# Performance work log

Hardware: AMD Instinct MI355X
Metric: run time of the kernel (lower is better)

The kernel has to match this reference:

```python
import jax, jax.numpy as jnp
import numpy as np

N = 50000
E = 800000
IN_DIM = 256
HID = 256
OUT_DIM = 2


def setup_inputs() -> dict:
    key = jax.random.key(0)
    ks = jax.random.split(key, 10)
    x = jax.random.normal(ks[0], (N, IN_DIM), dtype=jnp.float32)
    edge_index = jax.random.randint(ks[1], (2, E), 0, N, dtype=jnp.int64)
    # Glorot-ish scaling so activations stay well-conditioned through 4 layers
    def w(k, fan_in, fan_out):
        return jax.random.normal(k, (fan_in, fan_out), dtype=jnp.float32) / jnp.sqrt(jnp.float32(fan_in))
    return {
        "x": x,
        "edge_index": edge_index,
        "W0": w(ks[2], IN_DIM, HID), "b0": jnp.zeros((HID,), jnp.float32),
        "W1": w(ks[3], HID, HID),    "b1": jnp.zeros((HID,), jnp.float32),
        "W2": w(ks[4], HID, HID),    "b2": jnp.zeros((HID,), jnp.float32),
        "W3": w(ks[5], HID, OUT_DIM), "b3": jnp.zeros((OUT_DIM,), jnp.float32),
    }


def _gcn_norm(edge_index, n, dtype):
    # PyG gcn_norm with self-loops: deg over destination, norm = d^-1/2[src]*d^-1/2[dst]
    loops = jnp.arange(n, dtype=edge_index.dtype)
    src = jnp.concatenate([edge_index[0], loops])
    dst = jnp.concatenate([edge_index[1], loops])
    deg = jax.ops.segment_sum(jnp.ones_like(dst, dtype=dtype), dst, num_segments=n)
    dis = deg ** -0.5  # deg >= 1 due to self-loops
    norm = dis[src] * dis[dst]
    return src, dst, norm


def reference(x, edge_index, W0, b0, W1, b1, W2, b2, W3, b3):
    n = x.shape[0]
    src, dst, norm = _gcn_norm(edge_index, n, x.dtype)

    def conv(h, W, b):
        h = h @ W                              # [N, F_out] dense GEMM
        msg = h[src] * norm[:, None]           # edge-gather + scale
        agg = jax.ops.segment_sum(msg, dst, num_segments=n)  # scatter-add
        return agg + b

    h = jax.nn.relu(conv(x, W0, b0))
    h = jax.nn.relu(conv(h, W1, b1))
    h = jax.nn.relu(conv(h, W2, b2))
    return conv(h, W3, b3)
```

## Files before the change

kernel.cpp:

```cpp
#include <hip/hip_runtime.h>

#define N_NODES 50000
#define N_EDGES 800000

static inline int cdiv(int a, int b) { return (a + b - 1) / b; }

typedef __attribute__((ext_vector_type(8))) short bf16x8;
typedef __attribute__((ext_vector_type(4))) float f32x4;

static __device__ __forceinline__ unsigned short f2bf(float f) {
    unsigned int u = __float_as_uint(f);
    unsigned int r = (u + 0x7FFF + ((u >> 16) & 1)) >> 16;
    return (unsigned short)r;
}
static __device__ __forceinline__ float bf2f(unsigned short h) {
    return __uint_as_float((unsigned int)h << 16);
}
static __device__ __forceinline__ float bf_lo(unsigned int u) { return __uint_as_float(u << 16); }
static __device__ __forceinline__ float bf_hi(unsigned int u) { return __uint_as_float(u & 0xFFFF0000u); }

static __device__ __forceinline__ int logc(int p) {
    int pl = p & 63;
    return (p & ~63) + (pl & 3) * 16 + (pl >> 2);
}

static __device__ __forceinline__ void acc8(float* acc, uint4 v, float wgt) {
    acc[0] += wgt * bf_lo(v.x);
    acc[1] += wgt * bf_hi(v.x);
    acc[2] += wgt * bf_lo(v.y);
    acc[3] += wgt * bf_hi(v.y);
    acc[4] += wgt * bf_lo(v.z);
    acc[5] += wgt * bf_hi(v.z);
    acc[6] += wgt * bf_lo(v.w);
    acc[7] += wgt * bf_hi(v.w);
}


__global__ void k_init_cnt(int* cnt, int n) {
    int i = blockIdx.x * 256 + threadIdx.x;
    if (i < n) cnt[i] = 1;
}

__global__ void k_count(const int* __restrict__ edst, int* cnt, int e) {
    int i = blockIdx.x * 256 + threadIdx.x;
    if (i < e) atomicAdd(&cnt[edst[i]], 1);
}

__global__ __launch_bounds__(256) void k_scan1(const int* __restrict__ cnt,
                                               int* __restrict__ row_ptr,
                                               float* __restrict__ dis,
                                               int* __restrict__ blk, int n) {
    __shared__ int sums[256];
    int t = threadIdx.x;
    int base = blockIdx.x * 1024 + t * 4;
    int c0 = 0, c1 = 0, c2 = 0, c3 = 0;
    if (base + 3 < n) {
        int4 v = *(const int4*)(cnt + base);
        c0 = v.x; c1 = v.y; c2 = v.z; c3 = v.w;
    } else {
        if (base + 0 < n) c0 = cnt[base + 0];
        if (base + 1 < n) c1 = cnt[base + 1];
        if (base + 2 < n) c2 = cnt[base + 2];
        if (base + 3 < n) c3 = cnt[base + 3];
    }
    int s = c0 + c1 + c2 + c3;
    sums[t] = s;
    __syncthreads();
    int x = s;
    for (int off = 1; off < 256; off <<= 1) {
        int y = (t >= off) ? sums[t - off] : 0;
        __syncthreads();
        x += y;
        sums[t] = x;
        __syncthreads();
    }
    int excl = x - s;
    if (base + 0 < n) { row_ptr[base + 0] = excl;                dis[base + 0] = rsqrtf((float)c0); }
    if (base + 1 < n) { row_ptr[base + 1] = excl + c0;           dis[base + 1] = rsqrtf((float)c1); }
    if (base + 2 < n) { row_ptr[base + 2] = excl + c0 + c1;      dis[base + 2] = rsqrtf((float)c2); }
    if (base + 3 < n) { row_ptr[base + 3] = excl + c0 + c1 + c2; dis[base + 3] = rsqrtf((float)c3); }
    if (t == 255) blk[blockIdx.x] = x;
}

__global__ __launch_bounds__(256) void k_scan2(int* __restrict__ blk,
                                               int* __restrict__ row_ptr_n, int nb) {
    __shared__ int sums[256];
    int t = threadIdx.x;
    int s = (t < nb) ? blk[t] : 0;
    sums[t] = s;
    __syncthreads();
    int x = s;
    for (int off = 1; off < 256; off <<= 1) {
        int y = (t >= off) ? sums[t - off] : 0;
        __syncthreads();
        x += y;
        sums[t] = x;
        __syncthreads();
    }
    if (t < nb) blk[t] = x - s;
    if (t == 255) row_ptr_n[0] = x;
}

__global__ __launch_bounds__(256) void k_scan3(int* __restrict__ row_ptr,
                                               int* __restrict__ pos,
                                               const int* __restrict__ blk, int n) {
    int base = blockIdx.x * 1024 + threadIdx.x * 4;
    int off = blk[blockIdx.x];
#pragma unroll
    for (int i = 0; i < 4; ++i) {
        int idx = base + i;
        if (idx < n) {
            int v = row_ptr[idx] + off;
            row_ptr[idx] = v;
            pos[idx] = v;
        }
    }
}

__global__ void k_fill(const int* __restrict__ esrc, const int* __restrict__ edst,
                       int* pos, const float* __restrict__ dis,
                       int2* __restrict__ eg, int e, int n) {
    int i = blockIdx.x * 256 + threadIdx.x;
    if (i < e) {
        int s = esrc[i], d = edst[i];
        int p = atomicAdd(&pos[d], 1);
        eg[p] = make_int2(s, __float_as_int(dis[s] * dis[d]));
    } else if (i < e + n) {
        int v = i - e;
        int p = atomicAdd(&pos[v], 1);
        float dv = dis[v];
        eg[p] = make_int2(v, __float_as_int(dv * dv));
    }
}


__global__ __launch_bounds__(256) void k_split_w3(const float* __restrict__ W0,
                                                  const float* __restrict__ W1,
                                                  const float* __restrict__ W2,
                                                  unsigned short* __restrict__ Wth,
                                                  unsigned short* __restrict__ Wtl) {
    int layer = blockIdx.x >> 8;
    int n = blockIdx.x & 255;
    int p = threadIdx.x;
    const float* W = layer == 0 ? W0 : (layer == 1 ? W1 : W2);
    int k = (layer != 0) ? logc(p) : p;
    float v = W[(size_t)k * 256 + n];
    unsigned short h = f2bf(v);
    size_t o = (size_t)layer * 65536 + (size_t)n * 256 + p;
    Wth[o] = h;
    Wtl[o] = f2bf(v - bf2f(h));
}


__global__ __launch_bounds__(256) void k_cast_a(const float* __restrict__ X,
                                                unsigned short* __restrict__ Xh, long total4) {
    long i = (long)blockIdx.x * 256 + threadIdx.x;
    if (i >= total4) return;
    float4 v = *(const float4*)(X + i * 4);
    ushort4 h;
    h.x = f2bf(v.x);
    h.y = f2bf(v.y);
    h.z = f2bf(v.z);
    h.w = f2bf(v.w);
    *(ushort4*)(Xh + i * 4) = h;
}


#define GEMM_RB 196

__global__ __launch_bounds__(256) void k_gemm_mfma(const unsigned short* __restrict__ Ah,
                                                   const unsigned short* __restrict__ Wth,
                                                   const unsigned short* __restrict__ Wtl,
                                                   unsigned short* __restrict__ C, int M) {
    __shared__ unsigned short Wh[64][264];
    __shared__ unsigned short Wl[64][264];
    int rowblk = blockIdx.x % GEMM_RB;
    int colblk = blockIdx.x / GEMM_RB;
    int c0 = colblk * 64;
    int m0 = rowblk * 256;
    int t = threadIdx.x;

    {
        int r = t >> 2;
        int k0 = (t & 3) * 64;
        const unsigned short* gh = Wth + (size_t)(c0 + r) * 256 + k0;
        const unsigned short* gl = Wtl + (size_t)(c0 + r) * 256 + k0;
        unsigned short* lh = &Wh[r][k0];
        unsigned short* ll = &Wl[r][k0];
#pragma unroll
        for (int i = 0; i < 8; ++i) {
            *(uint4*)(lh + i * 8) = *(const uint4*)(gh + i * 8);
            *(uint4*)(ll + i * 8) = *(const uint4*)(gl + i * 8);
        }
    }
    __syncthreads();

    int lane = t & 63, wave = t >> 6;
    int quad = lane >> 4, l16 = lane & 15;

    const unsigned short* aph[4];
#pragma unroll
    for (int mt = 0; mt < 4; ++mt) {
        int m = m0 + wave * 64 + mt * 16 + l16;
        if (m >= M) m = M - 1;
        aph[mt] = Ah + (size_t)m * 256;
    }

    f32x4 acc[4][4];
#pragma unroll
    for (int i = 0; i < 4; ++i)
#pragma unroll
        for (int j = 0; j < 4; ++j) acc[i][j] = (f32x4){0.f, 0.f, 0.f, 0.f};

#pragma unroll 2
    for (int kc = 0; kc < 8; ++kc) {
        int ko = kc * 32 + quad * 8;
        bf16x8 ahf[4];
#pragma unroll
        for (int mt = 0; mt < 4; ++mt) ahf[mt] = *(const bf16x8*)(aph[mt] + ko);
#pragma unroll
        for (int nt = 0; nt < 4; ++nt) {
            bf16x8 bh = *(const bf16x8*)&Wh[nt * 16 + l16][ko];
            bf16x8 bl = *(const bf16x8*)&Wl[nt * 16 + l16][ko];
#pragma unroll
            for (int mt = 0; mt < 4; ++mt) {
                acc[mt][nt] = __builtin_amdgcn_mfma_f32_16x16x32_bf16(ahf[mt], bh, acc[mt][nt], 0, 0, 0);
                acc[mt][nt] = __builtin_amdgcn_mfma_f32_16x16x32_bf16(ahf[mt], bl, acc[mt][nt], 0, 0, 0);
            }
        }
    }

#pragma unroll
    for (int mt = 0; mt < 4; ++mt) {
#pragma unroll
        for (int r = 0; r < 4; ++r) {
            int row = m0 + wave * 64 + mt * 16 + quad * 4 + r;
            if (row < M) {
                ushort4 sv;
                sv.x = f2bf(acc[mt][0][r]);
                sv.y = f2bf(acc[mt][1][r]);
                sv.z = f2bf(acc[mt][2][r]);
                sv.w = f2bf(acc[mt][3][r]);
                *(ushort4*)(C + (size_t)row * 256 + c0 + l16 * 4) = sv;
            }
        }
    }
}


__global__ __launch_bounds__(256) void k_agg256(const unsigned short* __restrict__ t,
                                                const int* __restrict__ row_ptr,
                                                const int2* __restrict__ eg,
                                                const float* __restrict__ bias,
                                                unsigned short* __restrict__ outh, int n) {
    int lane = threadIdx.x & 63;
    int wave = threadIdx.x >> 6;
    int node = blockIdx.x * 4 + wave;
    if (node >= n) return;
    int half = lane >> 5;
    int fl = lane & 31;
    int beg = row_ptr[node], end = row_ptr[node + 1];
    float acc[8] = {};
    const unsigned short* tp = t + fl * 8;

    int e = beg + half;
    int2 m0, m1, m2, m3;
    bool have4 = (e + 6 < end);
    if (have4) { m0 = eg[e]; m1 = eg[e + 2]; m2 = eg[e + 4]; m3 = eg[e + 6]; }
    while (have4) {
        int en = e + 8;
        bool next4 = (en + 6 < end);
        int2 q0, q1, q2, q3;
        if (next4) { q0 = eg[en]; q1 = eg[en + 2]; q2 = eg[en + 4]; q3 = eg[en + 6]; }
        uint4 v0 = *(const uint4*)(tp + (size_t)m0.x * 256);
        uint4 v1 = *(const uint4*)(tp + (size_t)m1.x * 256);
        uint4 v2 = *(const uint4*)(tp + (size_t)m2.x * 256);
        uint4 v3 = *(const uint4*)(tp + (size_t)m3.x * 256);
        acc8(acc, v0, __int_as_float(m0.y));
        acc8(acc, v1, __int_as_float(m1.y));
        acc8(acc, v2, __int_as_float(m2.y));
        acc8(acc, v3, __int_as_float(m3.y));
        m0 = q0; m1 = q1; m2 = q2; m3 = q3;
        e = en;
        have4 = next4;
    }
    for (; e + 2 < end; e += 4) {
        int2 a = eg[e], b = eg[e + 2];
        uint4 v0 = *(const uint4*)(tp + (size_t)a.x * 256);
        uint4 v1 = *(const uint4*)(tp + (size_t)b.x * 256);
        acc8(acc, v0, __int_as_float(a.y));
        acc8(acc, v1, __int_as_float(b.y));
    }
    if (e < end) {
        int2 a = eg[e];
        uint4 v0 = *(const uint4*)(tp + (size_t)a.x * 256);
        acc8(acc, v0, __int_as_float(a.y));
    }

#pragma unroll
    for (int i = 0; i < 8; ++i) acc[i] += __shfl_xor(acc[i], 32);

    if (half == 0) {
        ushort4 h0, h1;
#pragma unroll
        for (int j = 0; j < 8; ++j) {
            int cb = logc(fl * 8 + j);
            float v = acc[j] + bias[cb];
            v = v > 0.f ? v : 0.f;
            unsigned short h = f2bf(v);
            if (j == 0) h0.x = h;
            else if (j == 1) h0.y = h;
            else if (j == 2) h0.z = h;
            else if (j == 3) h0.w = h;
            else if (j == 4) h1.x = h;
            else if (j == 5) h1.y = h;
            else if (j == 6) h1.z = h;
            else h1.w = h;
        }
        unsigned short* oh = outh + (size_t)node * 256 + fl * 8;
        *(ushort4*)(oh + 0) = h0;
        *(ushort4*)(oh + 4) = h1;
    }
}


__global__ __launch_bounds__(256) void k_gemm_out2(const unsigned short* __restrict__ Hh,
                                                   const float* __restrict__ W3,
                                                   float* __restrict__ t2, int n) {
    int lane = threadIdx.x & 63;
    int wave = threadIdx.x >> 6;
    int row = blockIdx.x * 4 + wave;
    if (row >= n) return;
    ushort4 ah = *(const ushort4*)(Hh + (size_t)row * 256 + lane * 4);
    float v[4];
    v[0] = bf2f(ah.x);
    v[1] = bf2f(ah.y);
    v[2] = bf2f(ah.z);
    v[3] = bf2f(ah.w);
    float s0 = 0.f, s1 = 0.f;
#pragma unroll
    for (int i = 0; i < 4; ++i) {
        int c = logc(lane * 4 + i);
        float2 w = *(const float2*)(W3 + (size_t)c * 2);
        s0 += v[i] * w.x;
        s1 += v[i] * w.y;
    }
#pragma unroll
    for (int off = 32; off > 0; off >>= 1) {
        s0 += __shfl_down(s0, off);
        s1 += __shfl_down(s1, off);
    }
    if (lane == 0) {
        t2[(size_t)row * 2 + 0] = s0;
        t2[(size_t)row * 2 + 1] = s1;
    }
}

__global__ void k_agg2(const float* __restrict__ t2,
                       const int* __restrict__ row_ptr,
                       const int2* __restrict__ eg,
                       const float* __restrict__ b3,
                       float* __restrict__ out, int n) {
    int node = blockIdx.x * 256 + threadIdx.x;
    if (node >= n) return;
    int beg = row_ptr[node], end = row_ptr[node + 1];
    float a0 = 0.f, a1 = 0.f;
    for (int e = beg; e < end; ++e) {
        int2 m = eg[e];
        float w = __int_as_float(m.y);
        float2 v = *(const float2*)(t2 + (size_t)m.x * 2);
        a0 += w * v.x;
        a1 += w * v.y;
    }
    out[(size_t)node * 2 + 0] = a0 + b3[0];
    out[(size_t)node * 2 + 1] = a1 + b3[1];
}


extern "C" void kernel_launch(void* const* d_in, const int* in_sizes, int n_in,
                              void* d_out, int out_size, void* d_ws, size_t ws_size,
                              hipStream_t stream) {
    const int N = N_NODES, E = N_EDGES;
    const float* x  = (const float*)d_in[0];
    const int* ei   = (const int*)d_in[1];
    const int* esrc = ei;
    const int* edst = ei + E;
    const float* W0 = (const float*)d_in[2];
    const float* b0 = (const float*)d_in[3];
    const float* W1 = (const float*)d_in[4];
    const float* b1 = (const float*)d_in[5];
    const float* W2 = (const float*)d_in[6];
    const float* b2 = (const float*)d_in[7];
    const float* W3 = (const float*)d_in[8];
    const float* b3 = (const float*)d_in[9];
    float* out = (float*)d_out;

    unsigned short* Ahh = (unsigned short*)d_ws;
    unsigned short* Tb  = Ahh + (size_t)N * 256;
    unsigned short* Wth = Tb + (size_t)N * 256;
    unsigned short* Wtl = Wth + 3 * 65536;
    int2*  eg     = (int2*)(Wtl + 3 * 65536);
    float* t2     = (float*)(eg + (E + N));
    float* dis    = t2 + (size_t)N * 2;
    int*   cnt    = (int*)(dis + N);
    int*   row_ptr= cnt + N;
    int*   pos    = row_ptr + (N + 1);
    int*   blk    = pos + N;

    const int NB = cdiv(N, 1024);

    k_init_cnt<<<cdiv(N, 256), 256, 0, stream>>>(cnt, N);
    k_count<<<cdiv(E, 256), 256, 0, stream>>>(edst, cnt, E);
    k_scan1<<<NB, 256, 0, stream>>>(cnt, row_ptr, dis, blk, N);
    k_scan2<<<1, 256, 0, stream>>>(blk, row_ptr + N, NB);
    k_scan3<<<NB, 256, 0, stream>>>(row_ptr, pos, blk, N);
    k_fill<<<cdiv(E + N, 256), 256, 0, stream>>>(esrc, edst, pos, dis, eg, E, N);

    const int ggrid = GEMM_RB * 4;
    const int agrid = cdiv(N, 4);
    const long total4 = (long)N * 64;

    k_cast_a<<<cdiv((int)total4, 256), 256, 0, stream>>>(x, Ahh, total4);
    k_split_w3<<<768, 256, 0, stream>>>(W0, W1, W2, Wth, Wtl);

    k_gemm_mfma<<<ggrid, 256, 0, stream>>>(Ahh, Wth, Wtl, Tb, N);
    k_agg256<<<agrid, 256, 0, stream>>>(Tb, row_ptr, eg, b0, Ahh, N);
    k_gemm_mfma<<<ggrid, 256, 0, stream>>>(Ahh, Wth + 65536, Wtl + 65536, Tb, N);
    k_agg256<<<agrid, 256, 0, stream>>>(Tb, row_ptr, eg, b1, Ahh, N);
    k_gemm_mfma<<<ggrid, 256, 0, stream>>>(Ahh, Wth + 2 * 65536, Wtl + 2 * 65536, Tb, N);
    k_agg256<<<agrid, 256, 0, stream>>>(Tb, row_ptr, eg, b2, Ahh, N);
    k_gemm_out2<<<agrid, 256, 0, stream>>>(Ahh, W3, t2, N);
    k_agg2<<<cdiv(N, 256), 256, 0, stream>>>(t2, row_ptr, eg, b3, out, N);
}
```

Before: 481.6 us.

## Merge prep kernels, memset counts, prefetch GEMM A fragments, simplify gather loop

Replaces the count-init kernel with a memset and adds the self-loop +1 inside the scan. Merges the weight-split and input-cast kernels into one launch. In the GEMM, the first A fragment load is issued before the LDS barrier, the k-loop is fully unrolled, and the next A fragment is software-prefetched. The aggregation loop drops its manual edge-metadata prefetch in favour of a plain unrolled loop. Together these aim to cut launch overhead and hide load latency, at the cost of more register pressure in the GEMM and possibly less latency hiding in the gather.

Result: no change. 480.6 us (-0.2%).

```diff
diff --git a/kernel.cpp b/kernel.cpp
--- a/kernel.cpp
+++ b/kernel.cpp
@@ -35,11 +35,6 @@
     acc[7] += wgt * bf_hi(v.w);
 }
 
-
-__global__ void k_init_cnt(int* cnt, int n) {
-    int i = blockIdx.x * 256 + threadIdx.x;
-    if (i < n) cnt[i] = 1;
-}
 
 __global__ void k_count(const int* __restrict__ edst, int* cnt, int e) {
     int i = blockIdx.x * 256 + threadIdx.x;
@@ -56,12 +51,12 @@
     int c0 = 0, c1 = 0, c2 = 0, c3 = 0;
     if (base + 3 < n) {
         int4 v = *(const int4*)(cnt + base);
-        c0 = v.x; c1 = v.y; c2 = v.z; c3 = v.w;
+        c0 = v.x + 1; c1 = v.y + 1; c2 = v.z + 1; c3 = v.w + 1;
     } else {
-        if (base + 0 < n) c0 = cnt[base + 0];
-        if (base + 1 < n) c1 = cnt[base + 1];
-        if (base + 2 < n) c2 = cnt[base + 2];
-        if (base + 3 < n) c3 = cnt[base + 3];
+        if (base + 0 < n) c0 = cnt[base + 0] + 1;
+        if (base + 1 < n) c1 = cnt[base + 1] + 1;
+        if (base + 2 < n) c2 = cnt[base + 2] + 1;
+        if (base + 3 < n) c3 = cnt[base + 3] + 1;
     }
     int s = c0 + c1 + c2 + c3;
     sums[t] = s;
@@ -134,35 +129,35 @@
 }
 
 
-__global__ __launch_bounds__(256) void k_split_w3(const float* __restrict__ W0,
-                                                  const float* __restrict__ W1,
-                                                  const float* __restrict__ W2,
-                                                  unsigned short* __restrict__ Wth,
-                                                  unsigned short* __restrict__ Wtl) {
-    int layer = blockIdx.x >> 8;
-    int n = blockIdx.x & 255;
-    int p = threadIdx.x;
-    const float* W = layer == 0 ? W0 : (layer == 1 ? W1 : W2);
-    int k = (layer != 0) ? logc(p) : p;
-    float v = W[(size_t)k * 256 + n];
-    unsigned short h = f2bf(v);
-    size_t o = (size_t)layer * 65536 + (size_t)n * 256 + p;
-    Wth[o] = h;
-    Wtl[o] = f2bf(v - bf2f(h));
-}
-
-
-__global__ __launch_bounds__(256) void k_cast_a(const float* __restrict__ X,
-                                                unsigned short* __restrict__ Xh, long total4) {
-    long i = (long)blockIdx.x * 256 + threadIdx.x;
-    if (i >= total4) return;
-    float4 v = *(const float4*)(X + i * 4);
-    ushort4 h;
-    h.x = f2bf(v.x);
-    h.y = f2bf(v.y);
-    h.z = f2bf(v.z);
-    h.w = f2bf(v.w);
-    *(ushort4*)(Xh + i * 4) = h;
+__global__ __launch_bounds__(256) void k_prep(const float* __restrict__ W0,
+                                              const float* __restrict__ W1,
+                                              const float* __restrict__ W2,
+                                              unsigned short* __restrict__ Wth,
+                                              unsigned short* __restrict__ Wtl,
+                                              const float* __restrict__ X,
+                                              unsigned short* __restrict__ Xh, long total4) {
+    if (blockIdx.x < 768) {
+        int layer = blockIdx.x >> 8;
+        int n = blockIdx.x & 255;
+        int p = threadIdx.x;
+        const float* W = layer == 0 ? W0 : (layer == 1 ? W1 : W2);
+        int k = (layer != 0) ? logc(p) : p;
+        float v = W[(size_t)k * 256 + n];
+        unsigned short h = f2bf(v);
+        size_t o = (size_t)layer * 65536 + (size_t)n * 256 + p;
+        Wth[o] = h;
+        Wtl[o] = f2bf(v - bf2f(h));
+    } else {
+        long i = (long)(blockIdx.x - 768) * 256 + threadIdx.x;
+        if (i >= total4) return;
+        float4 v = *(const float4*)(X + i * 4);
+        ushort4 h;
+        h.x = f2bf(v.x);
+        h.y = f2bf(v.y);
+        h.z = f2bf(v.z);
+        h.w = f2bf(v.w);
+        *(ushort4*)(Xh + i * 4) = h;
+    }
 }
 
 
@@ -193,7 +188,6 @@
             *(uint4*)(ll + i * 8) = *(const uint4*)(gl + i * 8);
         }
     }
-    __syncthreads();
 
     int lane = t & 63, wave = t >> 6;
     int quad = lane >> 4, l16 = lane & 15;
@@ -203,8 +197,14 @@
     for (int mt = 0; mt < 4; ++mt) {
         int m = m0 + wave * 64 + mt * 16 + l16;
         if (m >= M) m = M - 1;
-        aph[mt] = Ah + (size_t)m * 256;
-    }
+        aph[mt] = Ah + (size_t)m * 256 + quad * 8;
+    }
+
+    bf16x8 ahf[4];
+#pragma unroll
+    for (int mt = 0; mt < 4; ++mt) ahf[mt] = *(const bf16x8*)(aph[mt]);
+
+    __syncthreads();
 
     f32x4 acc[4][4];
 #pragma unroll
@@ -212,12 +212,14 @@
 #pragma unroll
         for (int j = 0; j < 4; ++j) acc[i][j] = (f32x4){0.f, 0.f, 0.f, 0.f};
 
-#pragma unroll 2
+#pragma unroll
     for (int kc = 0; kc < 8; ++kc) {
         int ko = kc * 32 + quad * 8;
-        bf16x8 ahf[4];
-#pragma unroll
-        for (int mt = 0; mt < 4; ++mt) ahf[mt] = *(const bf16x8*)(aph[mt] + ko);
+        bf16x8 nxt[4];
+        if (kc < 7) {
+#pragma unroll
+            for (int mt = 0; mt < 4; ++mt) nxt[mt] = *(const bf16x8*)(aph[mt] + (kc + 1) * 32);
+        }
 #pragma unroll
         for (int nt = 0; nt < 4; ++nt) {
             bf16x8 bh = *(const bf16x8*)&Wh[nt * 16 + l16][ko];
@@ -227,6 +229,10 @@
                 acc[mt][nt] = __builtin_amdgcn_mfma_f32_16x16x32_bf16(ahf[mt], bh, acc[mt][nt], 0, 0, 0);
                 acc[mt][nt] = __builtin_amdgcn_mfma_f32_16x16x32_bf16(ahf[mt], bl, acc[mt][nt], 0, 0, 0);
             }
+        }
+        if (kc < 7) {
+#pragma unroll
+            for (int mt = 0; mt < 4; ++mt) ahf[mt] = nxt[mt];
         }
     }
 
@@ -264,25 +270,16 @@
     const unsigned short* tp = t + fl * 8;
 
     int e = beg + half;
-    int2 m0, m1, m2, m3;
-    bool have4 = (e + 6 < end);
-    if (have4) { m0 = eg[e]; m1 = eg[e + 2]; m2 = eg[e + 4]; m3 = eg[e + 6]; }
-    while (have4) {
-        int en = e + 8;
-        bool next4 = (en + 6 < end);
-        int2 q0, q1, q2, q3;
-        if (next4) { q0 = eg[en]; q1 = eg[en + 2]; q2 = eg[en + 4]; q3 = eg[en + 6]; }
-        uint4 v0 = *(const uint4*)(tp + (size_t)m0.x * 256);
-        uint4 v1 = *(const uint4*)(tp + (size_t)m1.x * 256);
-        uint4 v2 = *(const uint4*)(tp + (size_t)m2.x * 256);
-        uint4 v3 = *(const uint4*)(tp + (size_t)m3.x * 256);
-        acc8(acc, v0, __int_as_float(m0.y));
-        acc8(acc, v1, __int_as_float(m1.y));
-        acc8(acc, v2, __int_as_float(m2.y));
-        acc8(acc, v3, __int_as_float(m3.y));
-        m0 = q0; m1 = q1; m2 = q2; m3 = q3;
-        e = en;
-        have4 = next4;
+    for (; e + 6 < end; e += 8) {
+        int2 a = eg[e], b = eg[e + 2], c = eg[e + 4], d = eg[e + 6];
+        uint4 v0 = *(const uint4*)(tp + (size_t)a.x * 256);
+        uint4 v1 = *(const uint4*)(tp + (size_t)b.x * 256);
+        uint4 v2 = *(const uint4*)(tp + (size_t)c.x * 256);
+        uint4 v3 = *(const uint4*)(tp + (size_t)d.x * 256);
+        acc8(acc, v0, __int_as_float(a.y));
+        acc8(acc, v1, __int_as_float(b.y));
+        acc8(acc, v2, __int_as_float(c.y));
+        acc8(acc, v3, __int_as_float(d.y));
     }
     for (; e + 2 < end; e += 4) {
         int2 a = eg[e], b = eg[e + 2];
@@ -409,7 +406,7 @@
 
     const int NB = cdiv(N, 1024);
 
-    k_init_cnt<<<cdiv(N, 256), 256, 0, stream>>>(cnt, N);
+    hipMemsetAsync(cnt, 0, (size_t)N * sizeof(int), stream);
     k_count<<<cdiv(E, 256), 256, 0, stream>>>(edst, cnt, E);
     k_scan1<<<NB, 256, 0, stream>>>(cnt, row_ptr, dis, blk, N);
     k_scan2<<<1, 256, 0, stream>>>(blk, row_ptr + N, NB);
@@ -419,9 +416,9 @@
     const int ggrid = GEMM_RB * 4;
     const int agrid = cdiv(N, 4);
     const long total4 = (long)N * 64;
-
-    k_cast_a<<<cdiv((int)total4, 256), 256, 0, stream>>>(x, Ahh, total4);
-    k_split_w3<<<768, 256, 0, stream>>>(W0, W1, W2, Wth, Wtl);
+    const int CA = cdiv((int)total4, 256);
+
+    k_prep<<<768 + CA, 256, 0, stream>>>(W0, W1, W2, Wth, Wtl, x, Ahh, total4);
 
     k_gemm_mfma<<<ggrid, 256, 0, stream>>>(Ahh, Wth, Wtl, Tb, N);
     k_agg256<<<agrid, 256, 0, stream>>>(Tb, row_ptr, eg, b0, Ahh, N);
```
